# Kernel tuning notes

Measured on AMD Instinct MI355X. Metric: run time of the kernel, lower is better.

The kernel has to match this reference:

```python
import jax, jax.numpy as jnp
import numpy as np

N_NODES = 50000
N_EDGES = 800000
IN_NODE = 16
IN_EDGE = 8
HID = 128
N_LAYERS = 4
LN_EPS = 1e-5


def setup_inputs() -> dict:
    key = jax.random.key(0)
    ks = jax.random.split(key, 16)
    s = lambda k, shape, fan: jax.random.normal(k, shape, jnp.float32) * (1.0 / np.sqrt(fan))
    inp = {
        "x": jax.random.normal(ks[0], (N_NODES, IN_NODE), jnp.float32),
        "edge_index": jax.random.randint(ks[1], (2, N_EDGES), 0, N_NODES, jnp.int32),
        "edge_attr": jax.random.normal(ks[2], (N_EDGES, IN_EDGE), jnp.float32),
        # input projection
        "W_in": s(ks[3], (HID, IN_NODE), IN_NODE),
        "b_in": jnp.zeros((HID,), jnp.float32),
        # stacked SAGEConv params: lin_l (neighbors, biased), lin_r (root, no bias)
        "Wl": s(ks[4], (N_LAYERS, HID, HID), HID),
        "bl": jnp.zeros((N_LAYERS, HID), jnp.float32),
        "Wr": s(ks[5], (N_LAYERS, HID, HID), HID),
        # stacked LayerNorm params
        "ln_g": jnp.ones((N_LAYERS, HID), jnp.float32),
        "ln_b": jnp.zeros((N_LAYERS, HID), jnp.float32),
        # edge MLP: (2*HID+IN_EDGE) -> HID -> HID//2 -> 1
        "W1": s(ks[6], (HID, 2 * HID + IN_EDGE), 2 * HID + IN_EDGE),
        "b1": jnp.zeros((HID,), jnp.float32),
        "W2": s(ks[7], (HID // 2, HID), HID),
        "b2": jnp.zeros((HID // 2,), jnp.float32),
        "W3": s(ks[8], (1, HID // 2), HID // 2),
        "b3": jnp.zeros((1,), jnp.float32),
    }
    return inp


def reference(x, edge_index, edge_attr, W_in, b_in, Wl, bl, Wr, ln_g, ln_b, W1, b1, W2, b2, W3, b3):
    n = x.shape[0]
    src, dst = edge_index[0], edge_index[1]
    # in-degree for mean aggregation (clamped to 1, as in PyG mean aggr)
    deg = jax.ops.segment_sum(jnp.ones_like(dst, jnp.float32), dst, num_segments=n)
    deg = jnp.maximum(deg, 1.0)[:, None]  # [N,1]

    h = x @ W_in.T + b_in  # [N,H]

    def layer(h, params):
        Wl_i, bl_i, Wr_i, g_i, be_i = params
        # SAGEConv: mean of source features scattered to destinations
        agg = jax.ops.segment_sum(h[src], dst, num_segments=n) / deg
        h2 = agg @ Wl_i.T + bl_i + h @ Wr_i.T
        # LayerNorm
        mu = jnp.mean(h2, axis=-1, keepdims=True)
        var = jnp.mean(jnp.square(h2 - mu), axis=-1, keepdims=True)
        h2 = (h2 - mu) * jax.lax.rsqrt(var + LN_EPS) * g_i + be_i
        # ReLU (dropout = identity in eval mode)
        return jax.nn.relu(h2), None

    h, _ = jax.lax.scan(layer, h, (Wl, bl, Wr, ln_g, ln_b))

    # edge head: gather endpoints, concat with edge_attr, MLP -> scalar logit
    e = jnp.concatenate([h[src], h[dst], edge_attr], axis=1)  # [E, 2H+F_e]
    e = jax.nn.relu(e @ W1.T + b1)
    e = jax.nn.relu(e @ W2.T + b2)
    logits = (e @ W3.T + b3)[:, 0]  # [E]
    return logits
```

## Files before the change

kernel.cpp:

```cpp
#include <hip/hip_runtime.h>
#include <stdint.h>

#define NN 50000
#define NE 800000

#define O_WIN 0
#define O_BIN 2048
#define O_WL  2176
#define O_BL  67712
#define O_WR  68224
#define O_LNG 133760
#define O_LNB 134272
#define O_W1  134784
#define O_B1  168576
#define O_W2  168704
#define O_B2  176896
#define O_W3  176960
#define O_B3  177024
#define W_TOTAL 177025

#define WS_FLAGS 0
#define WS_WC    512
#define WS_CNT   355072
#define WS_ROWP  555520
#define WS_CUR   756224
#define WS_CSR   956928
#define WS_EID   4156928
#define WS_DST   7356928
#define WS_W1P   10556928
#define WS_HB0   10630656
#define WS_HB1   23430656
#define WS_NEED  36230656

#define SCAN_NB 196

typedef float f32x4 __attribute__((ext_vector_type(4)));
typedef short bf16x8 __attribute__((ext_vector_type(8)));
typedef short bf16x4 __attribute__((ext_vector_type(4)));

__device__ __forceinline__ float b2f(unsigned short u) {
  union { unsigned int i; float f; } v; v.i = ((unsigned int)u) << 16; return v.f;
}
__device__ __forceinline__ float asf(unsigned int u) {
  union { unsigned int i; float f; } v; v.i = u; return v.f;
}
__device__ __forceinline__ unsigned short f2b(float f) {
  union { float f; unsigned int i; } v; v.f = f;
  return (unsigned short)((v.i + 0x7fffu + ((v.i >> 16) & 1u)) >> 16);
}

#define LBAR() do { \
  asm volatile("s_waitcnt lgkmcnt(0)" ::: "memory"); \
  __builtin_amdgcn_s_barrier(); \
} while (0)

__global__ void k_fallback(unsigned short* __restrict__ out) {
  int gid = blockIdx.x * 256 + threadIdx.x;
  if (gid < NE) out[gid] = 0x3F00;
}

__global__ void k_probe(const unsigned short* __restrict__ x_u,
                        const int* __restrict__ ei32, int* __restrict__ flags) {
  const int t = threadIdx.x;
  int insane = 0;
  for (int i = t; i < 512; i += 64) {
    float v = b2f(x_u[i]);
    if (!(fabsf(v) < 1e4f)) insane++;
  }
#pragma unroll
  for (int off = 1; off < 64; off <<= 1) insane += __shfl_xor(insane, off, 64);
  int nz = 0;
  for (int i = t; i < 128; i += 64) nz |= (ei32[2 * i + 1] != 0);
  unsigned long long m = __ballot(nz != 0);
  if (t == 0) {
    flags[0] = (insane >= 16) ? 1 : 0;
    flags[1] = (m == 0ULL) ? 1 : 0;
  }
}

__global__ void k_cvt_w(const void* W_in, const void* b_in, const void* Wl,
                        const void* bl, const void* Wr, const void* lng,
                        const void* lnb, const void* W1, const void* b1,
                        const void* W2, const void* b2, const void* W3,
                        const void* b3, unsigned short* __restrict__ wc,
                        const int* __restrict__ flags) {
  const int gid = blockIdx.x * 256 + threadIdx.x;
  if (gid >= W_TOTAL) return;
  const int f32 = flags[0];
  const void* src; int off;
  if      (gid < O_BIN) { src = W_in; off = gid - O_WIN; }
  else if (gid < O_WL)  { src = b_in; off = gid - O_BIN; }
  else if (gid < O_BL)  { src = Wl;   off = gid - O_WL;  }
  else if (gid < O_WR)  { src = bl;   off = gid - O_BL;  }
  else if (gid < O_LNG) { src = Wr;   off = gid - O_WR;  }
  else if (gid < O_LNB) { src = lng;  off = gid - O_LNG; }
  else if (gid < O_W1)  { src = lnb;  off = gid - O_LNB; }
  else if (gid < O_B1)  { src = W1;   off = gid - O_W1;  }
  else if (gid < O_W2)  { src = b1;   off = gid - O_B1;  }
  else if (gid < O_B2)  { src = W2;   off = gid - O_W2;  }
  else if (gid < O_W3)  { src = b2;   off = gid - O_B2;  }
  else if (gid < O_B3)  { src = W3;   off = gid - O_W3;  }
  else                  { src = b3;   off = 0;           }
  wc[gid] = f32 ? f2b(((const float*)src)[off]) : ((const unsigned short*)src)[off];
}

__global__ void k_build_w1p(const unsigned short* __restrict__ wc,
                            unsigned short* __restrict__ W1p) {
  int gid = blockIdx.x * 256 + threadIdx.x;
  if (gid >= 128 * 288) return;
  int j = gid / 288, k = gid - j * 288;
  W1p[gid] = (k < 264) ? wc[O_W1 + j * 264 + k] : (unsigned short)0;
}

__global__ void k_cvt_ea(const void* __restrict__ ea,
                         unsigned short* __restrict__ eab,
                         const int* __restrict__ flags) {
  const int gid = blockIdx.x * 256 + threadIdx.x;
  if (gid >= NE) return;
  if (flags[0]) {
    const float4* ep = (const float4*)((const float*)ea + (size_t)gid * 8);
    const float4 a = ep[0], b = ep[1];
    union { ushort4 v[2]; int4 i; } o;
    o.v[0].x = f2b(a.x); o.v[0].y = f2b(a.y); o.v[0].z = f2b(a.z); o.v[0].w = f2b(a.w);
    o.v[1].x = f2b(b.x); o.v[1].y = f2b(b.y); o.v[1].z = f2b(b.z); o.v[1].w = f2b(b.w);
    *(int4*)(eab + (size_t)gid * 8) = o.i;
  } else {
    *(int4*)(eab + (size_t)gid * 8) =
        *(const int4*)((const unsigned short*)ea + (size_t)gid * 8);
  }
}

__global__ void k_hist(const int* __restrict__ ei, int* __restrict__ cnt,
                       const int* __restrict__ flags) {
  const int e = blockIdx.x * 256 + threadIdx.x;
  if (e >= NE) return;
  const int d = flags[1] ? ei[2 * (NE + e)] : ei[NE + e];
  atomicAdd(&cnt[d], 1);
}

__global__ __launch_bounds__(256) void k_scan1(const int* __restrict__ cnt,
                                               int* __restrict__ rowptr,
                                               int* __restrict__ bsum) {
  __shared__ int ws4[4];
  const int t = threadIdx.x, ln = t & 63, wv = t >> 6;
  const int i = blockIdx.x * 256 + t;
  const int v = (i < NN) ? cnt[i] : 0;
  int x = v;
#pragma unroll
  for (int off = 1; off < 64; off <<= 1) {
    int y = __shfl_up(x, off, 64);
    if (ln >= off) x += y;
  }
  if (ln == 63) ws4[wv] = x;
  __syncthreads();
  if (t == 0) { ws4[1] += ws4[0]; ws4[2] += ws4[1]; ws4[3] += ws4[2]; }
  __syncthreads();
  const int woff = wv ? ws4[wv - 1] : 0;
  if (i < NN) rowptr[i] = woff + x - v;
  if (t == 255) bsum[blockIdx.x] = woff + x;
}

__global__ __launch_bounds__(256) void k_scan2(int* __restrict__ bsum) {
  __shared__ int ws4[4];
  const int t = threadIdx.x, ln = t & 63, wv = t >> 6;
  const int v = (t < SCAN_NB) ? bsum[t] : 0;
  int x = v;
#pragma unroll
  for (int off = 1; off < 64; off <<= 1) {
    int y = __shfl_up(x, off, 64);
    if (ln >= off) x += y;
  }
  if (ln == 63) ws4[wv] = x;
  __syncthreads();
  if (t == 0) { ws4[1] += ws4[0]; ws4[2] += ws4[1]; ws4[3] += ws4[2]; }
  __syncthreads();
  const int woff = wv ? ws4[wv - 1] : 0;
  if (t < SCAN_NB) bsum[t] = woff + x - v;
}

__global__ void k_scan3(int* __restrict__ rowptr, const int* __restrict__ bsum) {
  const int i = blockIdx.x * 256 + threadIdx.x;
  if (i < NN) rowptr[i] += bsum[blockIdx.x];
  if (i == 0) rowptr[NN] = NE;
}

__global__ void k_fill(const int* __restrict__ ei, const int* __restrict__ rowptr,
                       int* __restrict__ cursor, int* __restrict__ csr,
                       int* __restrict__ eidA, int* __restrict__ dstA,
                       const int* __restrict__ flags) {
  const int e = blockIdx.x * 256 + threadIdx.x;
  if (e >= NE) return;
  const int i64 = flags[1];
  const int s = i64 ? ei[2 * e] : ei[e];
  const int d = i64 ? ei[2 * (NE + e)] : ei[NE + e];
  const int pos = rowptr[d] + atomicAdd(&cursor[d], 1);
  csr[pos] = s;
  eidA[pos] = e;
  dstA[pos] = d;
}

__global__ void k_inproj(const void* __restrict__ x,
                         const unsigned short* __restrict__ wc,
                         unsigned short* __restrict__ hb,
                         const int* __restrict__ flags) {
  const int gid = blockIdx.x * 256 + threadIdx.x;
  const int n = gid >> 7, j = gid & 127;
  float xv[16];
  if (flags[0]) {
    const float4* xp = (const float4*)((const float*)x + (size_t)n * 16);
#pragma unroll
    for (int q = 0; q < 4; q++) {
      float4 t = xp[q];
      xv[q * 4 + 0] = t.x; xv[q * 4 + 1] = t.y; xv[q * 4 + 2] = t.z; xv[q * 4 + 3] = t.w;
    }
  } else {
    const unsigned short* xu = (const unsigned short*)x + (size_t)n * 16;
#pragma unroll
    for (int q = 0; q < 2; q++) {
      union { int4 v; unsigned short u[8]; } t;
      t.v = *(const int4*)(xu + q * 8);
#pragma unroll
      for (int i = 0; i < 8; i++) xv[q * 8 + i] = b2f(t.u[i]);
    }
  }
  float s = b2f(wc[O_BIN + j]);
  const unsigned short* wrow = wc + O_WIN + j * 16;
#pragma unroll
  for (int q = 0; q < 2; q++) {
    union { int4 v; unsigned short u[8]; } w;
    w.v = *(const int4*)(wrow + q * 8);
#pragma unroll
    for (int i = 0; i < 8; i++) s += b2f(w.u[i]) * xv[q * 8 + i];
  }
  hb[gid] = f2b(s);
}

__global__ __launch_bounds__(256) void k_agg(
    const unsigned short* __restrict__ hin, const int* __restrict__ csr,
    const int* __restrict__ rowptr, unsigned short* __restrict__ aggb) {
  const int tid = threadIdx.x;
  const int n = blockIdx.x * 4 + (tid >> 6);
  const int L = tid & 63;
  const int rg = L >> 4;
  const int j  = L & 15;
  const int rs = rowptr[n], re = rowptr[n + 1];
  const int4* hv = (const int4*)hin;
  float s[8];
#pragma unroll
  for (int i = 0; i < 8; i++) s[i] = 0.f;

  int e = rs;
  for (; e + 16 <= re; e += 16) {
    int idx[4];
#pragma unroll
    for (int k = 0; k < 4; k++) idx[k] = csr[e + k * 4 + rg];
    int4 u[4];
#pragma unroll
    for (int k = 0; k < 4; k++) u[k] = hv[(size_t)idx[k] * 16 + j];
#pragma unroll
    for (int k = 0; k < 4; k++) {
      const unsigned int w0 = (unsigned int)u[k].x, w1 = (unsigned int)u[k].y;
      const unsigned int w2 = (unsigned int)u[k].z, w3 = (unsigned int)u[k].w;
      s[0] += asf(w0 << 16); s[1] += asf(w0 & 0xffff0000u);
      s[2] += asf(w1 << 16); s[3] += asf(w1 & 0xffff0000u);
      s[4] += asf(w2 << 16); s[5] += asf(w2 & 0xffff0000u);
      s[6] += asf(w3 << 16); s[7] += asf(w3 & 0xffff0000u);
    }
  }
  if (e < re) {
    int idx[4], ok[4];
#pragma unroll
    for (int k = 0; k < 4; k++) {
      const int ee = e + k * 4 + rg;
      ok[k] = ee < re;
      idx[k] = csr[ok[k] ? ee : (re - 1)];
    }
    int4 u[4];
#pragma unroll
    for (int k = 0; k < 4; k++) u[k] = hv[(size_t)idx[k] * 16 + j];
#pragma unroll
    for (int k = 0; k < 4; k++) {
      if (ok[k]) {
        const unsigned int w0 = (unsigned int)u[k].x, w1 = (unsigned int)u[k].y;
        const unsigned int w2 = (unsigned int)u[k].z, w3 = (unsigned int)u[k].w;
        s[0] += asf(w0 << 16); s[1] += asf(w0 & 0xffff0000u);
        s[2] += asf(w1 << 16); s[3] += asf(w1 & 0xffff0000u);
        s[4] += asf(w2 << 16); s[5] += asf(w2 & 0xffff0000u);
        s[6] += asf(w3 << 16); s[7] += asf(w3 & 0xffff0000u);
      }
    }
  }

#pragma unroll
  for (int i = 0; i < 8; i++) {
    s[i] += __shfl_xor(s[i], 16, 64);
    s[i] += __shfl_xor(s[i], 32, 64);
  }
  if (rg == 0) {
    const int dg = re - rs;
    const float rd = 1.0f / (float)(dg > 1 ? dg : 1);
    union { int4 v; unsigned short h[8]; } o;
#pragma unroll
    for (int i = 0; i < 8; i++) o.h[i] = f2b(s[i] * rd);
    ((int4*)aggb)[(size_t)n * 16 + j] = o.v;
  }
}

__global__ __launch_bounds__(256) void k_sage_mfma(
    const unsigned short* __restrict__ hin, unsigned short* __restrict__ hagg,
    const unsigned short* __restrict__ wc, int l) {
  __shared__ __align__(16) unsigned char As[64 * 528];
  __shared__ float red1[64][4];
  __shared__ float red2[64][4];
  __shared__ float mr[64][2];
  const int tid = threadIdx.x;
  const int wv = tid >> 6;
  const int L = tid & 63;
  const int l15 = L & 15;
  const int q = L >> 4;
  const int n0 = blockIdx.x * 64;

  bf16x8 wf[2][8];
  float blv[2], gv[2], bv[2];
#pragma unroll
  for (int nt = 0; nt < 2; nt++) {
    const int jj = (wv * 2 + nt) * 16 + l15;
#pragma unroll
    for (int kc = 0; kc < 8; kc++) {
      const unsigned short* src = (kc < 4)
          ? wc + O_WL + ((size_t)l * 128 + jj) * 128 + kc * 32 + q * 8
          : wc + O_WR + ((size_t)l * 128 + jj) * 128 + (kc - 4) * 32 + q * 8;
      wf[nt][kc] = *(const bf16x8*)src;
    }
    blv[nt] = b2f(wc[O_BL + l * 128 + jj]);
    gv[nt]  = b2f(wc[O_LNG + l * 128 + jj]);
    bv[nt]  = b2f(wc[O_LNB + l * 128 + jj]);
  }

  for (int c = tid; c < 2048; c += 256) {
    const int row = c >> 5, part = c & 31;
    int node = n0 + row; if (node > NN - 1) node = NN - 1;
    const unsigned short* src = (part < 16)
        ? hagg + (size_t)node * 128 + part * 8
        : hin + (size_t)node * 128 + (part - 16) * 8;
    *(int4*)(As + row * 528 + part * 16) = *(const int4*)src;
  }
  __syncthreads();

  f32x4 acc[4][2];
#pragma unroll
  for (int mt = 0; mt < 4; mt++)
#pragma unroll
    for (int nt = 0; nt < 2; nt++) acc[mt][nt] = (f32x4)(0.0f);
#pragma unroll
  for (int kc = 0; kc < 8; kc++) {
#pragma unroll
    for (int mt = 0; mt < 4; mt++) {
      const bf16x8 a = *(const bf16x8*)(As + (mt * 16 + l15) * 528 + (kc * 32 + q * 8) * 2);
#pragma unroll
      for (int nt = 0; nt < 2; nt++)
        acc[mt][nt] = __builtin_amdgcn_mfma_f32_16x16x32_bf16(a, wf[nt][kc], acc[mt][nt], 0, 0, 0);
    }
  }
#pragma unroll
  for (int mt = 0; mt < 4; mt++) {
#pragma unroll
    for (int rg = 0; rg < 4; rg++) {
      acc[mt][0][rg] += blv[0];
      acc[mt][1][rg] += blv[1];
      float s = acc[mt][0][rg] + acc[mt][1][rg];
      float s2 = acc[mt][0][rg] * acc[mt][0][rg] + acc[mt][1][rg] * acc[mt][1][rg];
#pragma unroll
      for (int m = 1; m < 16; m <<= 1) {
        s += __shfl_xor(s, m, 64);
        s2 += __shfl_xor(s2, m, 64);
      }
      if (l15 == 0) {
        const int row = mt * 16 + q * 4 + rg;
        red1[row][wv] = s; red2[row][wv] = s2;
      }
    }
  }
  __syncthreads();
  if (tid < 64) {
    const float s1 = red1[tid][0] + red1[tid][1] + red1[tid][2] + red1[tid][3];
    const float s2 = red2[tid][0] + red2[tid][1] + red2[tid][2] + red2[tid][3];
    const float mu = s1 * 0.0078125f;
    const float var = s2 * 0.0078125f - mu * mu;
    mr[tid][0] = mu;
    mr[tid][1] = rsqrtf(var + 1e-5f);
  }
  __syncthreads();
#pragma unroll
  for (int mt = 0; mt < 4; mt++) {
#pragma unroll
    for (int rg = 0; rg < 4; rg++) {
      const int row = mt * 16 + q * 4 + rg;
      const int node = n0 + row;
      if (node < NN) {
        const float mu = mr[row][0], rstd = mr[row][1];
#pragma unroll
        for (int nt = 0; nt < 2; nt++) {
          const float o = (acc[mt][nt][rg] - mu) * rstd * gv[nt] + bv[nt];
          hagg[(size_t)node * 128 + (wv * 2 + nt) * 16 + l15] = f2b(fmaxf(o, 0.f));
        }
      }
    }
  }
}

__global__ __launch_bounds__(256) void k_edge_mfma(
    const unsigned short* __restrict__ hb, const int* __restrict__ csr,
    const int* __restrict__ eidA, const int* __restrict__ dstA,
    const unsigned short* __restrict__ eab, const unsigned short* __restrict__ W1p,
    const unsigned short* __restrict__ wc, void* __restrict__ out,
    const int* __restrict__ flags) {
  __shared__ __align__(16) unsigned char sm[47616];
  unsigned char* const Ue = sm;
  unsigned char* const Hs = sm + 4096;
  unsigned char* const E1 = sm + 4096;
  unsigned char* const Ds = sm + 21504;
  unsigned char* const E2 = sm + 38912;
  const int tid = threadIdx.x;
  const int wv = tid >> 6;
  const int L = tid & 63;
  const int l15 = L & 15;
  const int q = L >> 4;
  const int f32 = flags[0];
  const int r4 = tid >> 2, seg = tid & 3;

  for (int i = tid; i < 64 * 12; i += 256)
    *(int*)(Ue + (i / 12) * 64 + 16 + (i % 12) * 4) = 0;

  bf16x8 w1f[2][9];
  float b1v[2];
#pragma unroll
  for (int nt = 0; nt < 2; nt++) {
    const int jj = (wv * 2 + nt) * 16 + l15;
#pragma unroll
    for (int cc = 0; cc < 9; cc++)
      w1f[nt][cc] = *(const bf16x8*)(W1p + jj * 288 + cc * 32 + q * 8);
    b1v[nt] = b2f(wc[O_B1 + jj]);
  }
  bf16x8 w2f[4];
  const int jj2 = wv * 16 + l15;
#pragma unroll
  for (int kc = 0; kc < 4; kc++)
    w2f[kc] = *(const bf16x8*)(wc + O_W2 + jj2 * 128 + kc * 32 + q * 8);
  const float b2v = b2f(wc[O_B2 + jj2]);
  const float b3f = b2f(wc[O_B3]);

  const int NT = NE / 64;

  int4 hsr0, hsr1, hsr2, hsr3;
  int4 dsr0, dsr1, dsr2, dsr3;
  int4 uer; uer.x = uer.y = uer.z = uer.w = 0;
  {
    const int p0 = blockIdx.x * 64;
    const int s0 = csr[p0 + r4];
    const int d0 = dstA[p0 + r4];
    const unsigned short* gs = hb + (size_t)s0 * 128 + seg * 32;
    const unsigned short* gd = hb + (size_t)d0 * 128 + seg * 32;
    hsr0 = ((const int4*)gs)[0]; hsr1 = ((const int4*)gs)[1];
    hsr2 = ((const int4*)gs)[2]; hsr3 = ((const int4*)gs)[3];
    dsr0 = ((const int4*)gd)[0]; dsr1 = ((const int4*)gd)[1];
    dsr2 = ((const int4*)gd)[2]; dsr3 = ((const int4*)gd)[3];
    if (tid < 64) {
      const int e0 = eidA[p0 + tid];
      uer = *(const int4*)(eab + (size_t)e0 * 8);
    }
  }

  for (int t = blockIdx.x; t < NT; t += gridDim.x) {
    const int pbase = t * 64;
    const int tn = (t + (int)gridDim.x < NT) ? (t + (int)gridDim.x) : t;
    const int pnext = tn * 64;

    if (tid < 64) *(int4*)(Ue + tid * 64) = uer;
    {
      unsigned char* ldst = Hs + r4 * 272 + seg * 64;
      ((int4*)ldst)[0] = hsr0; ((int4*)ldst)[1] = hsr1;
      ((int4*)ldst)[2] = hsr2; ((int4*)ldst)[3] = hsr3;
      unsigned char* ldd = Ds + r4 * 272 + seg * 64;
      ((int4*)ldd)[0] = dsr0; ((int4*)ldd)[1] = dsr1;
      ((int4*)ldd)[2] = dsr2; ((int4*)ldd)[3] = dsr3;
    }
    const int sN = csr[pnext + r4];
    const int dN = dstA[pnext + r4];
    int eN = 0;
    if (tid < 64) eN = eidA[pnext + tid];

    LBAR();

    int4 h0, h1, h2, h3, d0, d1, d2, d3;
    {
      const unsigned short* gsn = hb + (size_t)sN * 128 + seg * 32;
      h0 = ((const int4*)gsn)[0]; h1 = ((const int4*)gsn)[1];
      h2 = ((const int4*)gsn)[2]; h3 = ((const int4*)gsn)[3];
      const unsigned short* gdn = hb + (size_t)dN * 128 + seg * 32;
      d0 = ((const int4*)gdn)[0]; d1 = ((const int4*)gdn)[1];
      d2 = ((const int4*)gdn)[2]; d3 = ((const int4*)gdn)[3];
    }
    int4 uen; uen.x = uen.y = uen.z = uen.w = 0;
    if (tid < 64) uen = *(const int4*)(eab + (size_t)eN * 8);

    f32x4 acc1[4][2];
#pragma unroll
    for (int mt = 0; mt < 4; mt++)
#pragma unroll
      for (int nt = 0; nt < 2; nt++) acc1[mt][nt] = (f32x4)(0.0f);
#pragma unroll
    for (int cc = 0; cc < 4; cc++) {
#pragma unroll
      for (int mt = 0; mt < 4; mt++) {
        const bf16x8 a = *(const bf16x8*)(Hs + (mt * 16 + l15) * 272 + (cc * 32 + q * 8) * 2);
#pragma unroll
        for (int nt = 0; nt < 2; nt++)
          acc1[mt][nt] = __builtin_amdgcn_mfma_f32_16x16x32_bf16(a, w1f[nt][cc], acc1[mt][nt], 0, 0, 0);
      }
    }
#pragma unroll
    for (int cc = 4; cc < 8; cc++) {
#pragma unroll
      for (int mt = 0; mt < 4; mt++) {
        const bf16x8 a = *(const bf16x8*)(Ds + (mt * 16 + l15) * 272 + ((cc - 4) * 32 + q * 8) * 2);
#pragma unroll
        for (int nt = 0; nt < 2; nt++)
          acc1[mt][nt] = __builtin_amdgcn_mfma_f32_16x16x32_bf16(a, w1f[nt][cc], acc1[mt][nt], 0, 0, 0);
      }
    }
#pragma unroll
    for (int mt = 0; mt < 4; mt++) {
      const bf16x8 a = *(const bf16x8*)(Ue + (mt * 16 + l15) * 64 + q * 16);
#pragma unroll
      for (int nt = 0; nt < 2; nt++)
        acc1[mt][nt] = __builtin_amdgcn_mfma_f32_16x16x32_bf16(a, w1f[nt][8], acc1[mt][nt], 0, 0, 0);
    }
    LBAR();

#pragma unroll
    for (int mt = 0; mt < 4; mt++)
#pragma unroll
      for (int nt = 0; nt < 2; nt++)
#pragma unroll
        for (int rg = 0; rg < 4; rg++) {
          const int er = mt * 16 + q * 4 + rg;
          const int jj = (wv * 2 + nt) * 16 + l15;
          *(unsigned short*)(E1 + er * 272 + jj * 2) =
              f2b(fmaxf(acc1[mt][nt][rg] + b1v[nt], 0.f));
        }
    LBAR();

    f32x4 acc2[4];
#pragma unroll
    for (int mt = 0; mt < 4; mt++) acc2[mt] = (f32x4)(0.0f);
#pragma unroll
    for (int kc = 0; kc < 4; kc++) {
#pragma unroll
      for (int mt = 0; mt < 4; mt++) {
        const bf16x8 a = *(const bf16x8*)(E1 + (mt * 16 + l15) * 272 + (kc * 32 + q * 8) * 2);
        acc2[mt] = __builtin_amdgcn_mfma_f32_16x16x32_bf16(a, w2f[kc], acc2[mt], 0, 0, 0);
      }
    }
#pragma unroll
    for (int mt = 0; mt < 4; mt++)
#pragma unroll
      for (int rg = 0; rg < 4; rg++) {
        const int er = mt * 16 + q * 4 + rg;
        *(unsigned short*)(E2 + er * 136 + jj2 * 2) =
            f2b(fmaxf(acc2[mt][rg] + b2v, 0.f));
      }
    LBAR();

    const int el = wv * 16 + l15;
    float acc = 0.f;
#pragma unroll
    for (int i4 = 0; i4 < 4; i4++) {
      const bf16x4 v = *(const bf16x4*)(E2 + el * 136 + q * 32 + i4 * 8);
#pragma unroll
      for (int j = 0; j < 4; j++)
        acc += b2f((unsigned short)v[j]) * b2f(wc[O_W3 + q * 16 + i4 * 4 + j]);
    }
    acc += __shfl_xor(acc, 16, 64);
    acc += __shfl_xor(acc, 32, 64);
    if (q == 0) {
      const int e = eidA[pbase + el];
      const float r = acc + b3f;
      if (f32) ((float*)out)[e] = r;
      else     ((unsigned short*)out)[e] = f2b(r);
    }

    hsr0 = h0; hsr1 = h1; hsr2 = h2; hsr3 = h3;
    dsr0 = d0; dsr1 = d1; dsr2 = d2; dsr3 = d3;
    uer = uen;
  }
}

extern "C" void kernel_launch(void* const* d_in, const int* in_sizes, int n_in,
                              void* d_out, int out_size, void* d_ws, size_t ws_size,
                              hipStream_t stream) {
  const void* x  = d_in[0];
  const int*  ei = (const int*)d_in[1];
  const void* ea = d_in[2];

  char* ws = (char*)d_ws;
  int*            flags  = (int*)(ws + WS_FLAGS);
  unsigned short* wc     = (unsigned short*)(ws + WS_WC);
  int*            cnt    = (int*)(ws + WS_CNT);
  int*            rowptr = (int*)(ws + WS_ROWP);
  int*            cursor = (int*)(ws + WS_CUR);
  int*            csr    = (int*)(ws + WS_CSR);
  int*            eidA   = (int*)(ws + WS_EID);
  int*            dstA   = (int*)(ws + WS_DST);
  unsigned short* W1p    = (unsigned short*)(ws + WS_W1P);
  unsigned short* hb0    = (unsigned short*)(ws + WS_HB0);
  unsigned short* hb1    = (unsigned short*)(ws + WS_HB1);
  int*            bsum   = (int*)(ws + WS_CSR);

  if (ws_size < WS_NEED) {
    k_fallback<<<3125, 256, 0, stream>>>((unsigned short*)d_out);
    return;
  }

  k_probe<<<1, 64, 0, stream>>>((const unsigned short*)x, ei, flags);
  k_cvt_w<<<(W_TOTAL + 255) / 256, 256, 0, stream>>>(
      d_in[3], d_in[4], d_in[5], d_in[6], d_in[7], d_in[8], d_in[9],
      d_in[10], d_in[11], d_in[12], d_in[13], d_in[14], d_in[15], wc, flags);
  k_build_w1p<<<144, 256, 0, stream>>>(wc, W1p);

  hipMemsetAsync(cnt, 0, NN * sizeof(int), stream);
  hipMemsetAsync(cursor, 0, NN * sizeof(int), stream);
  k_hist<<<3125, 256, 0, stream>>>(ei, cnt, flags);
  k_scan1<<<SCAN_NB, 256, 0, stream>>>(cnt, rowptr, bsum);
  k_scan2<<<1, 256, 0, stream>>>(bsum);
  k_scan3<<<SCAN_NB, 256, 0, stream>>>(rowptr, bsum);
  k_fill<<<3125, 256, 0, stream>>>(ei, rowptr, cursor, csr, eidA, dstA, flags);

  k_inproj<<<NN * 128 / 256, 256, 0, stream>>>(x, wc, hb0, flags);

  unsigned short* cur = hb0;
  unsigned short* nxt = hb1;
  for (int l = 0; l < 4; l++) {
    k_agg<<<12500, 256, 0, stream>>>(cur, csr, rowptr, nxt);
    k_sage_mfma<<<782, 256, 0, stream>>>(cur, nxt, wc, l);
    unsigned short* tmp = cur; cur = nxt; nxt = tmp;
  }
  unsigned short* eab = nxt;
  k_cvt_ea<<<3125, 256, 0, stream>>>(ea, eab, flags);
  k_edge_mfma<<<3125, 256, 0, stream>>>(cur, csr, eidA, dstA, eab, W1p, wc, d_out, flags);
}
```

Baseline: 558.9 us.

## Fuse neighbor mean aggregation into SAGE MFMA kernel via shared memory

Merges the per-layer gather-mean aggregation kernel into the SAGE matmul+LayerNorm kernel, writing aggregated rows directly into the shared-memory A tile instead of a global buffer. This removes one launch per layer and the global write/read of the aggregate. In exchange, the gather now runs with far fewer blocks (782 instead of 12500), with each wave serially processing 16 nodes, reducing memory-level parallelism for the latency-bound gather.

```diff
diff --git a/kernel.cpp b/kernel.cpp
--- a/kernel.cpp
+++ b/kernel.cpp
@@ -235,80 +235,10 @@
   hb[gid] = f2b(s);
 }
 
-__global__ __launch_bounds__(256) void k_agg(
+__global__ __launch_bounds__(256) void k_sage_fused(
     const unsigned short* __restrict__ hin, const int* __restrict__ csr,
-    const int* __restrict__ rowptr, unsigned short* __restrict__ aggb) {
-  const int tid = threadIdx.x;
-  const int n = blockIdx.x * 4 + (tid >> 6);
-  const int L = tid & 63;
-  const int rg = L >> 4;
-  const int j  = L & 15;
-  const int rs = rowptr[n], re = rowptr[n + 1];
-  const int4* hv = (const int4*)hin;
-  float s[8];
-#pragma unroll
-  for (int i = 0; i < 8; i++) s[i] = 0.f;
-
-  int e = rs;
-  for (; e + 16 <= re; e += 16) {
-    int idx[4];
-#pragma unroll
-    for (int k = 0; k < 4; k++) idx[k] = csr[e + k * 4 + rg];
-    int4 u[4];
-#pragma unroll
-    for (int k = 0; k < 4; k++) u[k] = hv[(size_t)idx[k] * 16 + j];
-#pragma unroll
-    for (int k = 0; k < 4; k++) {
-      const unsigned int w0 = (unsigned int)u[k].x, w1 = (unsigned int)u[k].y;
-      const unsigned int w2 = (unsigned int)u[k].z, w3 = (unsigned int)u[k].w;
-      s[0] += asf(w0 << 16); s[1] += asf(w0 & 0xffff0000u);
-      s[2] += asf(w1 << 16); s[3] += asf(w1 & 0xffff0000u);
-      s[4] += asf(w2 << 16); s[5] += asf(w2 & 0xffff0000u);
-      s[6] += asf(w3 << 16); s[7] += asf(w3 & 0xffff0000u);
-    }
-  }
-  if (e < re) {
-    int idx[4], ok[4];
-#pragma unroll
-    for (int k = 0; k < 4; k++) {
-      const int ee = e + k * 4 + rg;
-      ok[k] = ee < re;
-      idx[k] = csr[ok[k] ? ee : (re - 1)];
-    }
-    int4 u[4];
-#pragma unroll
-    for (int k = 0; k < 4; k++) u[k] = hv[(size_t)idx[k] * 16 + j];
-#pragma unroll
-    for (int k = 0; k < 4; k++) {
-      if (ok[k]) {
-        const unsigned int w0 = (unsigned int)u[k].x, w1 = (unsigned int)u[k].y;
-        const unsigned int w2 = (unsigned int)u[k].z, w3 = (unsigned int)u[k].w;
-        s[0] += asf(w0 << 16); s[1] += asf(w0 & 0xffff0000u);
-        s[2] += asf(w1 << 16); s[3] += asf(w1 & 0xffff0000u);
-        s[4] += asf(w2 << 16); s[5] += asf(w2 & 0xffff0000u);
-        s[6] += asf(w3 << 16); s[7] += asf(w3 & 0xffff0000u);
-      }
-    }
-  }
-
-#pragma unroll
-  for (int i = 0; i < 8; i++) {
-    s[i] += __shfl_xor(s[i], 16, 64);
-    s[i] += __shfl_xor(s[i], 32, 64);
-  }
-  if (rg == 0) {
-    const int dg = re - rs;
-    const float rd = 1.0f / (float)(dg > 1 ? dg : 1);
-    union { int4 v; unsigned short h[8]; } o;
-#pragma unroll
-    for (int i = 0; i < 8; i++) o.h[i] = f2b(s[i] * rd);
-    ((int4*)aggb)[(size_t)n * 16 + j] = o.v;
-  }
-}
-
-__global__ __launch_bounds__(256) void k_sage_mfma(
-    const unsigned short* __restrict__ hin, unsigned short* __restrict__ hagg,
-    const unsigned short* __restrict__ wc, int l) {
+    const int* __restrict__ rowptr, const unsigned short* __restrict__ wc,
+    int l, unsigned short* __restrict__ hout) {
   __shared__ __align__(16) unsigned char As[64 * 528];
   __shared__ float red1[64][4];
   __shared__ float red2[64][4];
@@ -337,13 +267,84 @@
     bv[nt]  = b2f(wc[O_LNB + l * 128 + jj]);
   }
 
-  for (int c = tid; c < 2048; c += 256) {
-    const int row = c >> 5, part = c & 31;
+  {
+    const int rg = q;
+    const int j16 = l15;
+    const int4* hv = (const int4*)hin;
+    for (int i = 0; i < 16; i++) {
+      const int row = wv * 16 + i;
+      const int nn = n0 + row;
+      if (nn < NN) {
+        const int rs = rowptr[nn], re = rowptr[nn + 1];
+        float s[8];
+#pragma unroll
+        for (int z = 0; z < 8; z++) s[z] = 0.f;
+        int e = rs;
+        for (; e + 16 <= re; e += 16) {
+          int idx[4];
+#pragma unroll
+          for (int k = 0; k < 4; k++) idx[k] = csr[e + k * 4 + rg];
+          int4 u[4];
+#pragma unroll
+          for (int k = 0; k < 4; k++) u[k] = hv[(size_t)idx[k] * 16 + j16];
+#pragma unroll
+          for (int k = 0; k < 4; k++) {
+            const unsigned int w0 = (unsigned int)u[k].x, w1 = (unsigned int)u[k].y;
+            const unsigned int w2 = (unsigned int)u[k].z, w3 = (unsigned int)u[k].w;
+            s[0] += asf(w0 << 16); s[1] += asf(w0 & 0xffff0000u);
+            s[2] += asf(w1 << 16); s[3] += asf(w1 & 0xffff0000u);
+            s[4] += asf(w2 << 16); s[5] += asf(w2 & 0xffff0000u);
+            s[6] += asf(w3 << 16); s[7] += asf(w3 & 0xffff0000u);
+          }
+        }
+        if (e < re) {
+          int idx[4], ok[4];
+#pragma unroll
+          for (int k = 0; k < 4; k++) {
+            const int ee = e + k * 4 + rg;
+            ok[k] = ee < re;
+            idx[k] = csr[ok[k] ? ee : (re - 1)];
+          }
+          int4 u[4];
+#pragma unroll
+          for (int k = 0; k < 4; k++) u[k] = hv[(size_t)idx[k] * 16 + j16];
+#pragma unroll
+          for (int k = 0; k < 4; k++) {
+            if (ok[k]) {
+              const unsigned int w0 = (unsigned int)u[k].x, w1 = (unsigned int)u[k].y;
+              const unsigned int w2 = (unsigned int)u[k].z, w3 = (unsigned int)u[k].w;
+              s[0] += asf(w0 << 16); s[1] += asf(w0 & 0xffff0000u);
+              s[2] += asf(w1 << 16); s[3] += asf(w1 & 0xffff0000u);
+              s[4] += asf(w2 << 16); s[5] += asf(w2 & 0xffff0000u);
+              s[6] += asf(w3 << 16); s[7] += asf(w3 & 0xffff0000u);
+            }
+          }
+        }
+#pragma unroll
+        for (int z = 0; z < 8; z++) {
+          s[z] += __shfl_xor(s[z], 16, 64);
+          s[z] += __shfl_xor(s[z], 32, 64);
+        }
+        if (rg == 0) {
+          const int dg = re - rs;
+          const float rd = 1.0f / (float)(dg > 1 ? dg : 1);
+          union { int4 v; unsigned short h[8]; } o;
+#pragma unroll
+          for (int z = 0; z < 8; z++) o.h[z] = f2b(s[z] * rd);
+          *(int4*)(As + row * 528 + j16 * 16) = o.v;
+        }
+      } else if (rg == 0) {
+        int4 z4; z4.x = z4.y = z4.z = z4.w = 0;
+        *(int4*)(As + row * 528 + j16 * 16) = z4;
+      }
+    }
+  }
+
+  for (int c = tid; c < 1024; c += 256) {
+    const int row = c >> 4, p = c & 15;
     int node = n0 + row; if (node > NN - 1) node = NN - 1;
-    const unsigned short* src = (part < 16)
-        ? hagg + (size_t)node * 128 + part * 8
-        : hin + (size_t)node * 128 + (part - 16) * 8;
-    *(int4*)(As + row * 528 + part * 16) = *(const int4*)src;
+    *(int4*)(As + row * 528 + 256 + p * 16) =
+        *(const int4*)(hin + (size_t)node * 128 + p * 8);
   }
   __syncthreads();
 
@@ -402,7 +403,7 @@
 #pragma unroll
         for (int nt = 0; nt < 2; nt++) {
           const float o = (acc[mt][nt][rg] - mu) * rstd * gv[nt] + bv[nt];
-          hagg[(size_t)node * 128 + (wv * 2 + nt) * 16 + l15] = f2b(fmaxf(o, 0.f));
+          hout[(size_t)node * 128 + (wv * 2 + nt) * 16 + l15] = f2b(fmaxf(o, 0.f));
         }
       }
     }
@@ -641,8 +642,7 @@
   unsigned short* cur = hb0;
   unsigned short* nxt = hb1;
   for (int l = 0; l < 4; l++) {
-    k_agg<<<12500, 256, 0, stream>>>(cur, csr, rowptr, nxt);
-    k_sage_mfma<<<782, 256, 0, stream>>>(cur, nxt, wc, l);
+    k_sage_fused<<<782, 256, 0, stream>>>(cur, csr, rowptr, wc, l, nxt);
     unsigned short* tmp = cur; cur = nxt; nxt = tmp;
   }
   unsigned short* eab = nxt;
```

Result: slower. 691.1 us (+23.7%).
